# Optimization experiments

Hardware: AMD Instinct MI355X
Metric: run time of the kernel (lower is better)

Reference implementation:

```python
import jax, jax.numpy as jnp
import numpy as np

NUM_CLASSES = 100  # static stand-in for int(max(label)+1)


def setup_inputs() -> dict:
    key = jax.random.key(0)
    k1, k2 = jax.random.split(key)
    feat = jax.random.normal(k1, (500000, 256), dtype=jnp.float32)
    label = jax.random.randint(k2, (500000,), 0, NUM_CLASSES, dtype=jnp.int64)
    return {"feat": feat, "label": label}


def reference(feat, label):
    # Per-class centers via segment mean (replaces the per-class python loop)
    counts = jax.ops.segment_sum(jnp.ones((feat.shape[0],), feat.dtype), label,
                                 num_segments=NUM_CLASSES)  # [C]
    centers = jax.ops.segment_sum(feat, label, num_segments=NUM_CLASSES)
    centers = centers / counts[:, None]  # [C, D]

    # ||f - c||_2 for all (sample, class) pairs without a [N, C, D] intermediate:
    # ||f||^2 - 2 f.c + ||c||^2
    sq_f = jnp.sum(feat * feat, axis=1, keepdims=True)          # [N, 1]
    sq_c = jnp.sum(centers * centers, axis=1)                    # [C]
    d2 = sq_f - 2.0 * (feat @ centers.T) + sq_c[None, :]         # [N, C]
    dist = jnp.sqrt(jnp.maximum(d2, 0.0))

    # distance of each sample to its own class center (margin=False branch)
    given = jnp.take_along_axis(dist, label[:, None], axis=1)[:, 0]  # [N]
    return given
```

## Files before the change

kernel.cpp:

```cpp
#include <hip/hip_runtime.h>
#include <math.h>

#define REALC  100
#define NCLASS 104
#define DIM    256
#define CPLANE (NCLASS * 64)

#define BLOCK  256
#define B1     1024
#define G1CH   128

#define SCALE    256.0f
#define INVSCALE (1.0f / 256.0f)

#define WS_SUMS    0
#define WS_COUNTS  (NCLASS * DIM)
#define WS_FLAG    (NCLASS * DIM + NCLASS)
#define WS_CENTERS (NCLASS * DIM + NCLASS + 4)

#define ZERO_N      (NCLASS * DIM + NCLASS)
#define ZERO_BLOCKS ((ZERO_N + BLOCK - 1) / BLOCK)

__global__ __launch_bounds__(BLOCK) void k0_init(int* __restrict__ zero_region,
                                                 int* __restrict__ flag,
                                                 const unsigned int* __restrict__ lab,
                                                 int n) {
    int b = blockIdx.x, t = threadIdx.x;
    if (b < ZERO_BLOCKS) {
        int idx = b * BLOCK + t;
        if (idx < ZERO_N) zero_region[idx] = 0;
    } else {
        __shared__ unsigned int any_nonzero;
        if (t == 0) any_nonzero = 0u;
        __syncthreads();
        unsigned int v = 0u;
        int limit = min(1024, (n - 1) / 2);
        for (int i = t; i < limit; i += BLOCK) v |= lab[2 * i + 1];
        if (v) atomicOr(&any_nonzero, 1u);
        __syncthreads();
        if (t == 0) *flag = (any_nonzero == 0u) ? 1 : 0;
    }
}

__global__ __launch_bounds__(B1, 4) void k1_accum(const float* __restrict__ feat,
                                                  const unsigned int* __restrict__ lab,
                                                  const int* __restrict__ flag,
                                                  int* __restrict__ sums,
                                                  int* __restrict__ counts,
                                                  int n) {
    __shared__ int lsum[2 * CPLANE];
    __shared__ int lcnt[NCLASS];
    int t = threadIdx.x, lane = t & 63, w = t >> 6;
    int chunk = blockIdx.x >> 1, half = blockIdx.x & 1;
    int is64 = *flag;

    for (int i = t; i < 2 * CPLANE; i += B1) lsum[i] = 0;
    if (t < NCLASS) lcnt[t] = 0;
    __syncthreads();

    int rpb = (n + G1CH - 1) / G1CH;
    int r0 = chunk * rpb, r1 = min(n, r0 + rpb);

    const float2* f2 = (const float2*)feat;
    int colbase = (half << 6) + lane;

    for (int bstart = r0 + (w << 6); bstart < r1; bstart += B1) {
        int jmax = min(64, r1 - bstart);
        int lv = 0;
        if (lane < jmax) {
            int idx = bstart + lane;
            int v = is64 ? (int)lab[2 * (size_t)idx] : (int)lab[idx];
            lv = min(max(v, 0), NCLASS - 1);
            if (half == 0) atomicAdd(&lcnt[lv], 1);
        }
        const float2* rp = f2 + (size_t)bstart * 128 + colbase;
        if (jmax == 64) {
#pragma unroll 16
            for (int j = 0; j < 64; j++) {
                int cls = __shfl(lv, j);
                float2 a = rp[(size_t)j * 128];
                int ix = __float2int_rn(a.x * SCALE);
                int iy = __float2int_rn(a.y * SCALE);
                atomicAdd(&lsum[(cls << 6) + lane], ix);
                atomicAdd(&lsum[CPLANE + (cls << 6) + lane], iy);
            }
        } else {
            for (int j = 0; j < jmax; j++) {
                int cls = __shfl(lv, j);
                float2 a = rp[(size_t)j * 128];
                int ix = __float2int_rn(a.x * SCALE);
                int iy = __float2int_rn(a.y * SCALE);
                atomicAdd(&lsum[(cls << 6) + lane], ix);
                atomicAdd(&lsum[CPLANE + (cls << 6) + lane], iy);
            }
        }
    }
    __syncthreads();

    int rot = (chunk & 31) * 416;
    for (int i = t; i < 2 * CPLANE; i += B1) {
        int ii = i + rot; if (ii >= 2 * CPLANE) ii -= 2 * CPLANE;
        int p = (ii >= CPLANE) ? 1 : 0;
        int r = ii - (p ? CPLANE : 0);
        int c = r >> 6, l = r & 63;
        int v = lsum[ii];
        if (v) atomicAdd(&sums[(c << 8) + (half << 7) + (l << 1) + p], v);
    }
    if (half == 0 && t < NCLASS) {
        int v = lcnt[t];
        if (v) atomicAdd(&counts[t], v);
    }
}

__global__ __launch_bounds__(BLOCK) void k2_centers(const int* __restrict__ sums,
                                                    const int* __restrict__ counts,
                                                    float* __restrict__ centers) {
    int idx = blockIdx.x * BLOCK + threadIdx.x;
    if (idx < NCLASS * DIM) {
        float cnt = (float)counts[idx >> 8];
        centers[idx] = ((float)sums[idx] * INVSCALE) / fmaxf(cnt, 1.0f);
    }
}

__global__ __launch_bounds__(BLOCK, 4) void k3_dist(const float* __restrict__ feat,
                                                    const unsigned int* __restrict__ lab,
                                                    const int* __restrict__ flag,
                                                    const float* __restrict__ centers,
                                                    float* __restrict__ out,
                                                    int n) {
    __shared__ float dbuf[4][64];
    int t = threadIdx.x, lane = t & 63, w = t >> 6;
    int base = (blockIdx.x * 4 + w) * 64;
    if (base >= n) return;
    int is64 = *flag;

    int idx = base + lane;
    int lv = 0;
    if (idx < n) {
        int v = is64 ? (int)lab[2 * (size_t)idx] : (int)lab[idx];
        lv = min(max(v, 0), NCLASS - 1);
    }

    const float4* f4 = (const float4*)feat;
    const float4* c4 = (const float4*)centers;
    int rend = min(64, n - base);

#pragma unroll 4
    for (int j = 0; j < rend; j++) {
        int cls = __shfl(lv, j);
        float4 r = f4[(size_t)(base + j) * 64 + lane];
        float4 c = c4[(size_t)cls * 64 + lane];
        float dx = r.x - c.x, dy = r.y - c.y, dz = r.z - c.z, dw = r.w - c.w;
        float p = dx * dx + dy * dy + dz * dz + dw * dw;
#pragma unroll
        for (int off = 32; off > 0; off >>= 1) p += __shfl_down(p, off);
        if (lane == 0) dbuf[w][j] = p;
    }
    if (lane < rend) out[base + lane] = sqrtf(dbuf[w][lane]);
}

extern "C" void kernel_launch(void* const* d_in, const int* in_sizes, int n_in,
                              void* d_out, int out_size, void* d_ws, size_t ws_size,
                              hipStream_t stream) {
    const float* feat = (const float*)d_in[0];
    const unsigned int* lab = (const unsigned int*)d_in[1];
    int n = in_sizes[0] / DIM;

    int* ws = (int*)d_ws;
    int* sums = ws + WS_SUMS;
    int* counts = ws + WS_COUNTS;
    int* flag = ws + WS_FLAG;
    float* centers = (float*)(ws + WS_CENTERS);
    float* out = (float*)d_out;

    k0_init<<<ZERO_BLOCKS + 1, BLOCK, 0, stream>>>(ws, flag, lab, n);

    k1_accum<<<G1CH * 2, B1, 0, stream>>>(feat, lab, flag, sums, counts, n);

    k2_centers<<<(NCLASS * DIM + BLOCK - 1) / BLOCK, BLOCK, 0, stream>>>(sums, counts, centers);

    int ntiles = (n + 63) >> 6;
    k3_dist<<<(ntiles + 3) >> 2, BLOCK, 0, stream>>>(feat, lab, flag, centers, out, n);
}
```

Measured before the change: 798.7 us.

## Write per-block partial sums and reduce separately; restructure distance loop per quarter-wave

Each k1 block now writes its full shared-memory partial table to a workspace buffer instead of issuing global atomics, and a new reduce kernel sums the 128 partials per element and computes the centers. This removes the global atomic contention and the separate zeroing of the sums region. The distance kernel now has each 16-lane group handle one row per iteration, using four float4 loads and a 4-step xor reduction instead of a 6-step shuffle reduction across all 64 lanes. The cost is roughly 13 MB of extra partial-sum traffic and a strided reduction pass.

```diff
diff --git a/kernel.cpp b/kernel.cpp
--- a/kernel.cpp
+++ b/kernel.cpp
@@ -5,6 +5,7 @@
 #define NCLASS 104
 #define DIM    256
 #define CPLANE (NCLASS * 64)
+#define TBL    (2 * CPLANE)
 
 #define BLOCK  256
 #define B1     1024
@@ -13,48 +14,41 @@
 #define SCALE    256.0f
 #define INVSCALE (1.0f / 256.0f)
 
-#define WS_SUMS    0
-#define WS_COUNTS  (NCLASS * DIM)
-#define WS_FLAG    (NCLASS * DIM + NCLASS)
-#define WS_CENTERS (NCLASS * DIM + NCLASS + 4)
-
-#define ZERO_N      (NCLASS * DIM + NCLASS)
-#define ZERO_BLOCKS ((ZERO_N + BLOCK - 1) / BLOCK)
-
-__global__ __launch_bounds__(BLOCK) void k0_init(int* __restrict__ zero_region,
+#define WS_COUNTS  0
+#define WS_FLAG    NCLASS
+#define WS_CENTERS 128
+#define WS_PART    (128 + NCLASS * DIM)
+
+__global__ __launch_bounds__(BLOCK) void k0_init(int* __restrict__ counts,
                                                  int* __restrict__ flag,
                                                  const unsigned int* __restrict__ lab,
                                                  int n) {
-    int b = blockIdx.x, t = threadIdx.x;
-    if (b < ZERO_BLOCKS) {
-        int idx = b * BLOCK + t;
-        if (idx < ZERO_N) zero_region[idx] = 0;
-    } else {
-        __shared__ unsigned int any_nonzero;
-        if (t == 0) any_nonzero = 0u;
-        __syncthreads();
-        unsigned int v = 0u;
-        int limit = min(1024, (n - 1) / 2);
-        for (int i = t; i < limit; i += BLOCK) v |= lab[2 * i + 1];
-        if (v) atomicOr(&any_nonzero, 1u);
-        __syncthreads();
-        if (t == 0) *flag = (any_nonzero == 0u) ? 1 : 0;
-    }
+    int t = threadIdx.x;
+    if (t < NCLASS) counts[t] = 0;
+    __shared__ unsigned int any_nonzero;
+    if (t == 0) any_nonzero = 0u;
+    __syncthreads();
+    unsigned int v = 0u;
+    int limit = min(1024, (n - 1) / 2);
+    for (int i = t; i < limit; i += BLOCK) v |= lab[2 * i + 1];
+    if (v) atomicOr(&any_nonzero, 1u);
+    __syncthreads();
+    if (t == 0) *flag = (any_nonzero == 0u) ? 1 : 0;
 }
 
 __global__ __launch_bounds__(B1, 4) void k1_accum(const float* __restrict__ feat,
                                                   const unsigned int* __restrict__ lab,
                                                   const int* __restrict__ flag,
-                                                  int* __restrict__ sums,
+                                                  int* __restrict__ part,
                                                   int* __restrict__ counts,
                                                   int n) {
-    __shared__ int lsum[2 * CPLANE];
+    __shared__ __align__(16) int lsum[TBL];
     __shared__ int lcnt[NCLASS];
     int t = threadIdx.x, lane = t & 63, w = t >> 6;
     int chunk = blockIdx.x >> 1, half = blockIdx.x & 1;
     int is64 = *flag;
 
-    for (int i = t; i < 2 * CPLANE; i += B1) lsum[i] = 0;
+    for (int i = t; i < TBL; i += B1) lsum[i] = 0;
     if (t < NCLASS) lcnt[t] = 0;
     __syncthreads();
 
@@ -97,29 +91,34 @@
     }
     __syncthreads();
 
-    int rot = (chunk & 31) * 416;
-    for (int i = t; i < 2 * CPLANE; i += B1) {
-        int ii = i + rot; if (ii >= 2 * CPLANE) ii -= 2 * CPLANE;
-        int p = (ii >= CPLANE) ? 1 : 0;
-        int r = ii - (p ? CPLANE : 0);
-        int c = r >> 6, l = r & 63;
-        int v = lsum[ii];
-        if (v) atomicAdd(&sums[(c << 8) + (half << 7) + (l << 1) + p], v);
-    }
+    int4* pb = (int4*)(part + (size_t)blockIdx.x * TBL);
+    const int4* ls = (const int4*)lsum;
+    for (int i = t; i < TBL / 4; i += B1) pb[i] = ls[i];
+
     if (half == 0 && t < NCLASS) {
         int v = lcnt[t];
         if (v) atomicAdd(&counts[t], v);
     }
 }
 
-__global__ __launch_bounds__(BLOCK) void k2_centers(const int* __restrict__ sums,
-                                                    const int* __restrict__ counts,
-                                                    float* __restrict__ centers) {
-    int idx = blockIdx.x * BLOCK + threadIdx.x;
-    if (idx < NCLASS * DIM) {
-        float cnt = (float)counts[idx >> 8];
-        centers[idx] = ((float)sums[idx] * INVSCALE) / fmaxf(cnt, 1.0f);
-    }
+__global__ __launch_bounds__(BLOCK) void k2_reduce(const int* __restrict__ part,
+                                                   const int* __restrict__ counts,
+                                                   float* __restrict__ centers) {
+    int i = blockIdx.x * BLOCK + threadIdx.x;
+    if (i >= NCLASS * DIM) return;
+    int h = (i >= TBL) ? 1 : 0;
+    int j = i - h * TBL;
+    const int* p0 = part + (size_t)h * TBL + j;
+    int acc = 0;
+#pragma unroll 8
+    for (int k = 0; k < G1CH; k++) acc += p0[(size_t)(2 * k) * TBL];
+
+    int p = (j >= CPLANE) ? 1 : 0;
+    int r = j - p * CPLANE;
+    int c = r >> 6, l = r & 63;
+    int col = (h << 7) + (l << 1) + p;
+    float cnt = (float)counts[c];
+    centers[c * DIM + col] = ((float)acc * INVSCALE) / fmaxf(cnt, 1.0f);
 }
 
 __global__ __launch_bounds__(BLOCK, 4) void k3_dist(const float* __restrict__ feat,
@@ -145,18 +144,43 @@
     const float4* c4 = (const float4*)centers;
     int rend = min(64, n - base);
 
-#pragma unroll 4
-    for (int j = 0; j < rend; j++) {
-        int cls = __shfl(lv, j);
-        float4 r = f4[(size_t)(base + j) * 64 + lane];
-        float4 c = c4[(size_t)cls * 64 + lane];
-        float dx = r.x - c.x, dy = r.y - c.y, dz = r.z - c.z, dw = r.w - c.w;
-        float p = dx * dx + dy * dy + dz * dz + dw * dw;
+    if (rend == 64) {
+        int g = lane >> 4, s = lane & 15;
+#pragma unroll 2
+        for (int i = 0; i < 16; i++) {
+            int r = 4 * i + g;
+            int cls = __shfl(lv, r);
+            const float4* fr = f4 + (size_t)(base + r) * 64 + s;
+            const float4* cr = c4 + (size_t)cls * 64 + s;
+            float p = 0.0f;
 #pragma unroll
-        for (int off = 32; off > 0; off >>= 1) p += __shfl_down(p, off);
-        if (lane == 0) dbuf[w][j] = p;
-    }
-    if (lane < rend) out[base + lane] = sqrtf(dbuf[w][lane]);
+            for (int k = 0; k < 4; k++) {
+                float4 a = fr[16 * k];
+                float4 c = cr[16 * k];
+                float dx = a.x - c.x, dy = a.y - c.y, dz = a.z - c.z, dw = a.w - c.w;
+                p = fmaf(dx, dx, p); p = fmaf(dy, dy, p);
+                p = fmaf(dz, dz, p); p = fmaf(dw, dw, p);
+            }
+            p += __shfl_xor(p, 1);
+            p += __shfl_xor(p, 2);
+            p += __shfl_xor(p, 4);
+            p += __shfl_xor(p, 8);
+            if (s == 0) dbuf[w][r] = p;
+        }
+        out[base + lane] = sqrtf(dbuf[w][lane]);
+    } else {
+        for (int j = 0; j < rend; j++) {
+            int cls = __shfl(lv, j);
+            float4 a = f4[(size_t)(base + j) * 64 + lane];
+            float4 c = c4[(size_t)cls * 64 + lane];
+            float dx = a.x - c.x, dy = a.y - c.y, dz = a.z - c.z, dw = a.w - c.w;
+            float p = fmaf(dx, dx, fmaf(dy, dy, fmaf(dz, dz, dw * dw)));
+#pragma unroll
+            for (int off = 32; off > 0; off >>= 1) p += __shfl_down(p, off);
+            if (lane == 0) dbuf[w][j] = p;
+        }
+        if (lane < rend) out[base + lane] = sqrtf(dbuf[w][lane]);
+    }
 }
 
 extern "C" void kernel_launch(void* const* d_in, const int* in_sizes, int n_in,
@@ -167,17 +191,17 @@
     int n = in_sizes[0] / DIM;
 
     int* ws = (int*)d_ws;
-    int* sums = ws + WS_SUMS;
     int* counts = ws + WS_COUNTS;
     int* flag = ws + WS_FLAG;
     float* centers = (float*)(ws + WS_CENTERS);
+    int* part = ws + WS_PART;
     float* out = (float*)d_out;
 
-    k0_init<<<ZERO_BLOCKS + 1, BLOCK, 0, stream>>>(ws, flag, lab, n);
-
-    k1_accum<<<G1CH * 2, B1, 0, stream>>>(feat, lab, flag, sums, counts, n);
-
-    k2_centers<<<(NCLASS * DIM + BLOCK - 1) / BLOCK, BLOCK, 0, stream>>>(sums, counts, centers);
+    k0_init<<<1, BLOCK, 0, stream>>>(counts, flag, lab, n);
+
+    k1_accum<<<G1CH * 2, B1, 0, stream>>>(feat, lab, flag, part, counts, n);
+
+    k2_reduce<<<(NCLASS * DIM + BLOCK - 1) / BLOCK, BLOCK, 0, stream>>>(part, counts, centers);
 
     int ntiles = (n + 63) >> 6;
     k3_dist<<<(ntiles + 3) >> 2, BLOCK, 0, stream>>>(feat, lab, flag, centers, out, n);
```

New measurement: 789.8 us. No clear change (-1.1%).
